# Performance work log

Measured on AMD Instinct MI355X. Metric: run time of the kernel, lower is better.

The kernel has to match this reference:

```python
import jax, jax.numpy as jnp
import numpy as np

EMBED, PDIM, HEADS, FFN = 192, 96, 8, 384
HID = int(2 * FFN / 3)                        # 256
CH = [HID - (HID // 4) * 3] + [HID // 4] * 3  # [64, 64, 64, 64]
SCALES = [1, 3, 5, 7]
B, H, W = 8, 128, 128


def conv2d(x, w, b=None, pad=0, groups=1):
    out = jax.lax.conv_general_dilated(
        x, w, (1, 1), [(pad, pad), (pad, pad)],
        feature_group_count=groups,
        dimension_numbers=('NCHW', 'OIHW', 'NCHW'))
    return out if b is None else out + b[None, :, None, None]


def layer_norm(x, g, b, eps=1e-6):
    m = x.mean(-1, keepdims=True)
    v = ((x - m) ** 2).mean(-1, keepdims=True)
    return (x - m) * jax.lax.rsqrt(v + eps) * g + b


def batch_norm(x, g, b, m, v, eps=1e-5):
    # eval-mode BatchNorm2d with running stats
    inv = jax.lax.rsqrt(v + eps)
    return (x - m[None, :, None, None]) * (g * inv)[None, :, None, None] + b[None, :, None, None]


def block_forward(x, p):
    # --- pos: depthwise 3x3 residual ---
    xc = x.transpose(0, 3, 1, 2)  # NCHW
    xc = xc + conv2d(xc, p['pos_w'], p['pos_b'], pad=1, groups=EMBED)

    # --- retention (ATK_SPA) branch ---
    y = layer_norm(xc.transpose(0, 2, 3, 1), p['ln1_g'], p['ln1_b'])
    yc = y.transpose(0, 3, 1, 2)
    b, c, h, w = yc.shape
    x1, x2 = yc[:, :PDIM], yc[:, PDIM:]
    qkv = conv2d(conv2d(x1, p['qkv_w']), p['qkv_dw_w'], pad=1, groups=3 * PDIM)
    q, k, v = jnp.split(qkv, 3, axis=1)
    cph = PDIM // HEADS
    rs = lambda t: t.reshape(b, HEADS, cph, h * w)
    q, k, v = rs(q), rs(k), rs(v)
    q = q / jnp.maximum(jnp.linalg.norm(q, axis=-1, keepdims=True), 1e-12)
    k = k / jnp.maximum(jnp.linalg.norm(k, axis=-1, keepdims=True), 1e-12)
    attn = jnp.einsum('bhcn,bhdn->bhcd', q, k) * p['temperature']  # [b,heads,cph,cph]
    # dynamic top-k from gate (int() truncation -> floor, value is positive)
    g1 = jax.nn.relu(conv2d(yc, p['gate_w1'], p['gate_b1']))
    gate = jax.nn.sigmoid(conv2d(g1, p['gate_w2'], p['gate_b2']))
    dyn_k = jnp.floor(cph * gate.mean())
    # rank-based top-k mask == scatter of topk indices (jit-safe for dynamic k)
    ranks = jnp.argsort(jnp.argsort(-attn, axis=-1), axis=-1)
    mask = ranks.astype(attn.dtype) < dyn_k
    attn = jax.nn.softmax(jnp.where(mask, attn, -jnp.inf), axis=-1)
    out = jnp.einsum('bhcd,bhdn->bhcn', attn, v)
    # out1..out4 are identical; weighted sum == single matmul scaled
    out = out * (p['attn1'] + p['attn2'] + p['attn3'] + p['attn4'])
    out = out.reshape(b, PDIM, h, w)
    out = conv2d(jnp.concatenate([out, x2], axis=1), p['proj_w'])
    xc = xc + out

    # --- FFN (HSSFGN) branch ---
    z = layer_norm(xc.transpose(0, 2, 3, 1), p['ln2_g'], p['ln2_b'])
    zc = z.transpose(0, 3, 1, 2)
    v0 = batch_norm(jax.nn.gelu(conv2d(zc, p['fc1_w']), approximate=False),
                    p['bn1_g'], p['bn1_b'], p['bn1_m'], p['bn1_v'])
    parts = jnp.split(v0, np.cumsum(CH[:-1]).tolist(), axis=1)
    dws = [conv2d(parts[i], p['dw%d_w' % i], p['dw%d_b' % i],
                  pad=SCALES[i] // 2, groups=CH[i]) for i in range(4)]
    u = jnp.concatenate(dws, axis=1) + v0
    u = batch_norm(jax.nn.gelu(u, approximate=False),
                   p['bn2_g'], p['bn2_b'], p['bn2_m'], p['bn2_v'])
    u = u * v0
    u = batch_norm(conv2d(u, p['fc2_w']),
                   p['bn3_g'], p['bn3_b'], p['bn3_m'], p['bn3_v'])
    xc = xc + u
    return xc.transpose(0, 2, 3, 1)


def setup_inputs() -> dict:
    ki = iter(jax.random.split(jax.random.key(0), 64))
    nrm = lambda shape, s=0.05: jax.random.normal(next(ki), shape, dtype=jnp.float32) * s
    inp = {
        'x': jax.random.normal(next(ki), (B, H, W, EMBED), dtype=jnp.float32),
        'pos_w': nrm((EMBED, 1, 3, 3)), 'pos_b': jnp.zeros((EMBED,)),
        'ln1_g': jnp.ones((EMBED,)), 'ln1_b': jnp.zeros((EMBED,)),
        'temperature': jnp.ones((HEADS, 1, 1)),
        'qkv_w': nrm((3 * PDIM, PDIM, 1, 1)),
        'qkv_dw_w': nrm((3 * PDIM, 1, 3, 3)),
        'proj_w': nrm((EMBED, EMBED, 1, 1)),
        'gate_w1': nrm((EMBED // 2, EMBED, 1, 1), 0.02), 'gate_b1': jnp.zeros((EMBED // 2,)),
        'gate_w2': nrm((1, EMBED // 2, 1, 1), 0.02), 'gate_b2': jnp.zeros((1,)),
        'attn1': jnp.full((1,), 0.2), 'attn2': jnp.full((1,), 0.2),
        'attn3': jnp.full((1,), 0.2), 'attn4': jnp.full((1,), 0.2),
        'ln2_g': jnp.ones((EMBED,)), 'ln2_b': jnp.zeros((EMBED,)),
        'fc1_w': nrm((HID, EMBED, 1, 1)),
        'bn1_g': jnp.ones((HID,)), 'bn1_b': jnp.zeros((HID,)),
        'bn1_m': jnp.zeros((HID,)), 'bn1_v': jnp.ones((HID,)),
        'bn2_g': jnp.ones((HID,)), 'bn2_b': jnp.zeros((HID,)),
        'bn2_m': jnp.zeros((HID,)), 'bn2_v': jnp.ones((HID,)),
        'fc2_w': nrm((EMBED, HID, 1, 1)),
        'bn3_g': jnp.ones((EMBED,)), 'bn3_b': jnp.zeros((EMBED,)),
        'bn3_m': jnp.zeros((EMBED,)), 'bn3_v': jnp.ones((EMBED,)),
    }
    for i in range(4):
        inp['dw%d_w' % i] = nrm((CH[i], 1, SCALES[i], SCALES[i]))
        inp['dw%d_b' % i] = jnp.zeros((CH[i],))
    return inp


def reference(x, pos_w, pos_b, ln1_g, ln1_b, temperature, qkv_w, qkv_dw_w, proj_w,
              gate_w1, gate_b1, gate_w2, gate_b2, attn1, attn2, attn3, attn4,
              ln2_g, ln2_b, fc1_w, bn1_g, bn1_b, bn1_m, bn1_v,
              dw0_w, dw0_b, dw1_w, dw1_b, dw2_w, dw2_b, dw3_w, dw3_b,
              bn2_g, bn2_b, bn2_m, bn2_v, fc2_w, bn3_g, bn3_b, bn3_m, bn3_v):
    p = dict(locals())
    xx = p.pop('x')
    return block_forward(xx, p)
```

## Files before the change

### kernel.cpp

```cpp
#include <hip/hip_runtime.h>
#include <hip/hip_bf16.h>
#include <math.h>

#define BB 8
#define HH 128
#define WW 128
#define HW (HH*WW)
#define NPIX (BB*HW)

typedef unsigned short u16;
typedef __attribute__((ext_vector_type(4))) float  floatx4;
typedef __attribute__((ext_vector_type(4))) short  short4v;
typedef __attribute__((ext_vector_type(8))) short  short8v;

static __device__ __forceinline__ float gelu_exact(float x){
    return 0.5f*x*(1.0f+erff(x*0.70710678118654752440f));
}
static __device__ __forceinline__ float b2f(u16 v){
    union { unsigned u; float f; } x; x.u = ((unsigned)v)<<16; return x.f;
}
static __device__ __forceinline__ u16 f2b(float f){
    __hip_bfloat16 h = __float2bfloat16(f);
    return *(u16*)&h;
}

#define WQ 27648
#define WP 36864
#define WG 18432
#define WF1 49152
#define WF2 49152
#define WTOT (WQ+WP+WG+WF1+WF2)
__global__ __launch_bounds__(256) void wprep_k(const float* __restrict__ a,
    const float* __restrict__ b, const float* __restrict__ c,
    const float* __restrict__ d, const float* __restrict__ e, u16* __restrict__ o)
{
    int i = blockIdx.x*256 + threadIdx.x;
    if (i >= WTOT) return;
    float v;
    if (i < WQ) v = a[i];
    else if (i < WQ+WP) v = b[i-WQ];
    else if (i < WQ+WP+WG) v = c[i-WQ-WP];
    else if (i < WQ+WP+WG+WF1) v = d[i-WQ-WP-WG];
    else v = e[i-WQ-WP-WG-WF1];
    o[i] = f2b(v);
}

__global__ __launch_bounds__(256) void pos_conv_k(const float* __restrict__ x,
    const float* __restrict__ w, const float* __restrict__ bias, u16* __restrict__ out)
{
    int bid = blockIdx.x;
    int sb = (bid & 7)*(gridDim.x >> 3) + (bid >> 3);
    int gid = sb*256 + threadIdx.x;
    int c4 = gid % 48; int rest = gid / 48;
    int seg = rest & 15; rest >>= 4;
    int hy = rest % HH; int b = rest / HH;
    int c0 = c4*4;
    float wr[3][3][4];
    #pragma unroll
    for (int j=0;j<4;j++)
        #pragma unroll
        for (int ky=0;ky<3;ky++)
            #pragma unroll
            for (int kx=0;kx<3;kx++)
                wr[ky][kx][j] = w[(c0+j)*9 + ky*3 + kx];
    float4 bias4 = *(const float4*)(bias + c0);
    const float4* x4 = (const float4*)x;
    const float4* r0 = x4 + ((size_t)(b*HH + hy-1)*WW)*48 + c4;
    const float4* r1 = x4 + ((size_t)(b*HH + hy  )*WW)*48 + c4;
    const float4* r2 = x4 + ((size_t)(b*HH + hy+1)*WW)*48 + c4;
    bool v0 = hy > 0, v2 = hy < HH-1;
    float4 z4 = make_float4(0.f,0.f,0.f,0.f);
    int s0 = seg*8;
    float4 cA[3], cB[3], cC[3], cP[3], cN[3];
    bool la = s0 > 0;
    cA[0] = (v0&&la) ? r0[(size_t)(s0-1)*48] : z4;
    cA[1] = la ? r1[(size_t)(s0-1)*48] : z4;
    cA[2] = (v2&&la) ? r2[(size_t)(s0-1)*48] : z4;
    cB[0] = v0 ? r0[(size_t)s0*48] : z4;  cB[1] = r1[(size_t)s0*48];  cB[2] = v2 ? r2[(size_t)s0*48] : z4;
    cC[0] = v0 ? r0[(size_t)(s0+1)*48] : z4; cC[1] = r1[(size_t)(s0+1)*48]; cC[2] = v2 ? r2[(size_t)(s0+1)*48] : z4;
    {
        bool ok = (s0+2) < WW;
        size_t off = (size_t)(s0+2)*48;
        cP[0] = (v0&&ok) ? r0[off] : z4;
        cP[1] = ok ? r1[off] : z4;
        cP[2] = (v2&&ok) ? r2[off] : z4;
    }
    u16* orow = out + ((size_t)(b*HH + hy)*WW)*192 + c0;
    for (int i2=0; i2<8; i2++){
        int wx = s0 + i2;
        bool okc = (wx+3) < WW;
        size_t noff = (size_t)(wx+3)*48;
        cN[0] = (v0 && okc) ? r0[noff] : z4;
        cN[1] = okc ? r1[noff] : z4;
        cN[2] = (v2 && okc) ? r2[noff] : z4;
        float4 acc = bias4;
        #pragma unroll
        for (int i=0;i<3;i++){
            acc.x = fmaf(wr[i][0][0], cA[i].x, acc.x);
            acc.y = fmaf(wr[i][0][1], cA[i].y, acc.y);
            acc.z = fmaf(wr[i][0][2], cA[i].z, acc.z);
            acc.w = fmaf(wr[i][0][3], cA[i].w, acc.w);
            acc.x = fmaf(wr[i][1][0], cB[i].x, acc.x);
            acc.y = fmaf(wr[i][1][1], cB[i].y, acc.y);
            acc.z = fmaf(wr[i][1][2], cB[i].z, acc.z);
            acc.w = fmaf(wr[i][1][3], cB[i].w, acc.w);
            acc.x = fmaf(wr[i][2][0], cC[i].x, acc.x);
            acc.y = fmaf(wr[i][2][1], cC[i].y, acc.y);
            acc.z = fmaf(wr[i][2][2], cC[i].z, acc.z);
            acc.w = fmaf(wr[i][2][3], cC[i].w, acc.w);
        }
        acc.x += cB[1].x; acc.y += cB[1].y; acc.z += cB[1].z; acc.w += cB[1].w;
        short4v o; o.x=(short)f2b(acc.x); o.y=(short)f2b(acc.y);
        o.z=(short)f2b(acc.z); o.w=(short)f2b(acc.w);
        *(short4v*)(orow + (size_t)wx*192) = o;
        #pragma unroll
        for (int i=0;i<3;i++){ cA[i]=cB[i]; cB[i]=cC[i]; cC[i]=cP[i]; cP[i]=cN[i]; }
    }
}

__global__ __launch_bounds__(256) void ln_k(const u16* __restrict__ in,
    const float* __restrict__ g, const float* __restrict__ bta, u16* __restrict__ out)
{
    int wid = threadIdx.x >> 6, lane = threadIdx.x & 63;
    size_t pix = (size_t)blockIdx.x*4 + wid;
    const u16* row = in + pix*192;
    float x0 = b2f(row[lane]), x1 = b2f(row[lane+64]), x2 = b2f(row[lane+128]);
    float s = x0+x1+x2;
    float q = x0*x0 + x1*x1 + x2*x2;
    #pragma unroll
    for (int off=32; off; off>>=1){ s += __shfl_xor(s,off,64); q += __shfl_xor(q,off,64); }
    float mean = s*(1.f/192.f);
    float var  = q*(1.f/192.f) - mean*mean;
    float inv  = rsqrtf(var + 1e-6f);
    u16* orow = out + pix*192;
    orow[lane]     = f2b((x0-mean)*inv*g[lane]     + bta[lane]);
    orow[lane+64]  = f2b((x1-mean)*inv*g[lane+64]  + bta[lane+64]);
    orow[lane+128] = f2b((x2-mean)*inv*g[lane+128] + bta[lane+128]);
}

#define GM_NONE 0
#define GM_RES 1
#define GM_GELU_BN 2
#define GM_BN_RES 3
#define GM_BIAS_RELU 4
#define WSTR 264

template<int MODE, int K, bool SPLIT=false>
__global__ __launch_bounds__(256) void gemm_bf16_k(
    const u16* __restrict__ A, int lda,
    const u16* __restrict__ A2, int lda2,
    const u16* __restrict__ W,
    void* __restrict__ Cv, int ldc,
    const u16* __restrict__ R, int ldr,
    const float* __restrict__ bg, const float* __restrict__ bb,
    const float* __restrict__ bm_, const float* __restrict__ bv,
    int N)
{
    __shared__ u16 Ws[64*WSTR];
    int t = threadIdx.x;
    int bn = blockIdx.x * 64;
    int bm = blockIdx.y * 256;
    {
        constexpr int KQ = K/4;
        int brow = t >> 2, bq = t & 3;
        int n = bn + brow;
        bool nv = n < N;
        const u16* src = W + (size_t)n*K + bq*KQ;
        #pragma unroll
        for (int j=0; j<KQ; j+=8){
            short8v v = {};
            if (nv) v = *(const short8v*)(src + j);
            *(short8v*)&Ws[brow*WSTR + bq*KQ + j] = v;
        }
    }
    __syncthreads();
    int wave = t >> 6, lane = t & 63;
    int wm = wave*64;
    int lr = lane & 15, lk = lane >> 4;
    const u16* arow  = A + (size_t)(bm + wm + lr)*lda + lk*8;
    const u16* arow2 = SPLIT ? (A2 + (size_t)(bm + wm + lr)*lda2 + lk*8) : nullptr;
    floatx4 acc[4][4] = {};
    #pragma unroll
    for (int k0 = 0; k0 < K; k0 += 32){
        short8v afr[4];
        if (SPLIT && k0 >= 96){
            #pragma unroll
            for (int m=0;m<4;m++)
                afr[m] = *(const short8v*)(arow2 + (size_t)(m*16)*lda2 + (k0-96));
        } else {
            #pragma unroll
            for (int m=0;m<4;m++)
                afr[m] = *(const short8v*)(arow + (size_t)(m*16)*lda + k0);
        }
        #pragma unroll
        for (int n2=0;n2<4;n2++){
            short8v bfr = *(const short8v*)&Ws[(n2*16+lr)*WSTR + k0 + lk*8];
            #pragma unroll
            for (int m=0;m<4;m++)
                acc[m][n2] = __builtin_amdgcn_mfma_f32_16x16x32_bf16(afr[m], bfr, acc[m][n2], 0,0,0);
        }
    }
    #pragma unroll
    for (int m=0;m<4;m++){
        #pragma unroll
        for (int n2=0;n2<4;n2++){
            int gcol = bn + n2*16 + lr;
            if (gcol >= N) continue;
            #pragma unroll
            for (int rg=0; rg<4; rg++){
                int grow = bm + wm + m*16 + lk*4 + rg;
                float v = acc[m][n2][rg];
                if (MODE == GM_RES){
                    v += b2f(R[(size_t)grow*ldr + gcol]);
                    ((u16*)Cv)[(size_t)grow*ldc + gcol] = f2b(v);
                } else if (MODE == GM_BN_RES){
                    float bnv = (v - bm_[gcol])*rsqrtf(bv[gcol]+1e-5f)*bg[gcol] + bb[gcol];
                    ((float*)Cv)[(size_t)grow*ldc + gcol] = bnv + b2f(R[(size_t)grow*ldr + gcol]);
                } else if (MODE == GM_GELU_BN){
                    float gl = gelu_exact(v);
                    v = (gl - bm_[gcol])*rsqrtf(bv[gcol]+1e-5f)*bg[gcol] + bb[gcol];
                    ((u16*)Cv)[(size_t)grow*ldc + gcol] = f2b(v);
                } else if (MODE == GM_BIAS_RELU){
                    ((u16*)Cv)[(size_t)grow*ldc + gcol] = f2b(fmaxf(v + bg[gcol], 0.f));
                } else {
                    ((u16*)Cv)[(size_t)grow*ldc + gcol] = f2b(v);
                }
            }
        }
    }
}

__global__ __launch_bounds__(256) void gate2_k(const u16* __restrict__ G1,
    const float* __restrict__ w2, const float* __restrict__ b2, float* __restrict__ gpix)
{
    int pix = blockIdx.x*256 + threadIdx.x;
    const short4v* g4 = (const short4v*)(G1 + (size_t)pix*96);
    const float4* w4 = (const float4*)w2;
    float s = b2[0];
    #pragma unroll
    for (int j=0;j<24;j++){
        short4v g = g4[j]; float4 w = w4[j];
        s += b2f((u16)g.x)*w.x + b2f((u16)g.y)*w.y + b2f((u16)g.z)*w.z + b2f((u16)g.w)*w.w;
    }
    gpix[pix] = 1.f/(1.f+expf(-s));
}

__global__ __launch_bounds__(1024) void gate_reduce_k(const float* __restrict__ gpix,
                                                      float* __restrict__ dynk)
{
    __shared__ float sm[16];
    float s = 0.f;
    for (int i=threadIdx.x; i<NPIX; i+=1024) s += gpix[i];
    #pragma unroll
    for (int off=32; off; off>>=1) s += __shfl_xor(s,off,64);
    int wid = threadIdx.x>>6, lane = threadIdx.x&63;
    if (lane==0) sm[wid]=s;
    __syncthreads();
    if (threadIdx.x==0){
        float tot=0.f; for (int i=0;i<16;i++) tot+=sm[i];
        *dynk = floorf(12.0f * (tot/(float)NPIX));
    }
}

#define QPOS(c8) ((c8)*8 + ((c8)>>2)*4)
#define QTAPSTRIDE 324
__global__ __launch_bounds__(256) void qkv_dw_k(const u16* __restrict__ in,
    const float* __restrict__ w, u16* __restrict__ out, size_t planeStride)
{
    __shared__ float wlds[9*QTAPSTRIDE];
    int t = threadIdx.x;
    for (int i=t; i<2592; i+=256){
        int tap = i/288, cc = i%288;
        wlds[tap*QTAPSTRIDE + QPOS(cc>>3) + (cc&7)] = w[cc*9+tap];
    }
    __syncthreads();
    int bid = blockIdx.x;
    int sb = (bid & 7)*(gridDim.x >> 3) + (bid >> 3);
    int idx = sb*256 + t;
    int c8 = idx % 36; int px2 = idx / 36;
    int wp = px2 & 63; int hy = (px2 >> 6) & 127; int img = px2 >> 13;
    int wx0 = wp*2;
    int c0 = c8*8;
    int wofs = QPOS(c8);
    float acc0[8] = {}, acc1[8] = {};
    #pragma unroll
    for (int ky=0; ky<3; ky++){
        int hh = hy + ky - 1; if ((unsigned)hh >= HH) continue;
        const u16* rowp = in + ((size_t)(img*HH+hh)*WW)*288 + c0;
        #pragma unroll
        for (int cc=0; cc<4; cc++){
            int cx = wx0 - 1 + cc;
            if ((unsigned)cx >= WW) continue;
            short8v v = *(const short8v*)(rowp + (size_t)cx*288);
            float vf[8];
            #pragma unroll
            for (int j=0;j<8;j++) vf[j] = b2f((u16)v[j]);
            if (cc < 3){
                floatx4 wa = *(const floatx4*)&wlds[(ky*3+cc)*QTAPSTRIDE + wofs];
                floatx4 wb = *(const floatx4*)&wlds[(ky*3+cc)*QTAPSTRIDE + wofs + 4];
                #pragma unroll
                for (int j=0;j<4;j++){ acc0[j]   = fmaf(wa[j], vf[j],   acc0[j]);
                                       acc0[4+j] = fmaf(wb[j], vf[4+j], acc0[4+j]); }
            }
            if (cc >= 1){
                floatx4 wa = *(const floatx4*)&wlds[(ky*3+cc-1)*QTAPSTRIDE + wofs];
                floatx4 wb = *(const floatx4*)&wlds[(ky*3+cc-1)*QTAPSTRIDE + wofs + 4];
                #pragma unroll
                for (int j=0;j<4;j++){ acc1[j]   = fmaf(wa[j], vf[j],   acc1[j]);
                                       acc1[4+j] = fmaf(wb[j], vf[4+j], acc1[4+j]); }
            }
        }
    }
    size_t pix0 = (size_t)(img*HH+hy)*WW + wx0;
    int sec = c0/96, qc0 = c0 - sec*96;
    u16* outp = out + (size_t)sec*planeStride + qc0;
    short8v o0, o1;
    #pragma unroll
    for (int j=0;j<8;j++){ o0[j] = (short)f2b(acc0[j]); o1[j] = (short)f2b(acc1[j]); }
    *(short8v*)(outp + pix0*96) = o0;
    *(short8v*)(outp + (pix0+1)*96) = o1;
}

__global__ __launch_bounds__(256) void gram_k(const u16* __restrict__ Qp,
    const u16* __restrict__ Kp, float* __restrict__ part)
{
    int bh = blockIdx.x;
    int slice = blockIdx.y;
    int img = bh >> 3, h = bh & 7;
    const u16* Qb = Qp + (size_t)img*HW*96 + h*12;
    const u16* Kb = Kp + (size_t)img*HW*96 + h*12;
    __shared__ float qs[64][12];
    __shared__ float ks[64][12];
    int t = threadIdx.x;
    float acc = 0.f;
    int c = (t<144) ? t/12 : (t<156 ? t-144 : t-156);
    int d = (t<144) ? t%12 : 0;
    for (int st=0; st<16; st++){
        int pix0 = slice*1024 + st*64;
        __syncthreads();
        for (int i=t; i<384; i+=256){
            int p = i/6, j = i%6;
            const u16* src = (j<3) ? (Qb + (size_t)(pix0+p)*96 + j*4)
                                   : (Kb + (size_t)(pix0+p)*96 + (j-3)*4);
            short4v v = *(const short4v*)src;
            float f0=b2f((u16)v.x), f1=b2f((u16)v.y), f2=b2f((u16)v.z), f3=b2f((u16)v.w);
            if (j<3){ int jj=j*4;     qs[p][jj]=f0; qs[p][jj+1]=f1; qs[p][jj+2]=f2; qs[p][jj+3]=f3; }
            else    { int jj=(j-3)*4; ks[p][jj]=f0; ks[p][jj+1]=f1; ks[p][jj+2]=f2; ks[p][jj+3]=f3; }
        }
        __syncthreads();
        if (t<144){        for (int p=0;p<64;p++) acc = fmaf(qs[p][c], ks[p][d], acc); }
        else if (t<156){   for (int p=0;p<64;p++) acc = fmaf(qs[p][c], qs[p][c], acc); }
        else if (t<168){   for (int p=0;p<64;p++) acc = fmaf(ks[p][c], ks[p][c], acc); }
    }
    if (t<168) part[((size_t)bh*16 + slice)*168 + t] = acc;
}

__global__ __launch_bounds__(256) void gram_combine_k(const float* __restrict__ part,
                                                      float* __restrict__ gram, int n)
{
    int i = blockIdx.x*256 + threadIdx.x;
    if (i >= n) return;
    int bh = i/168, t = i%168;
    float s = 0.f;
    for (int sl=0; sl<16; sl++) s += part[((size_t)bh*16+sl)*168 + t];
    gram[i] = s;
}

__global__ __launch_bounds__(256) void attn_k(const float* __restrict__ gram,
    const float* __restrict__ temp, const float* __restrict__ dynk_p,
    const float* __restrict__ a1, const float* __restrict__ a2,
    const float* __restrict__ a3, const float* __restrict__ a4,
    float* __restrict__ attnW)
{
    int bh = blockIdx.x;
    int h = bh & 7;
    __shared__ float av[12][12];
    __shared__ float mv[12][12];
    __shared__ float nq[12], nk[12];
    int t = threadIdx.x;
    if (t < 12) nq[t] = fmaxf(sqrtf(gram[bh*168+144+t]), 1e-12f);
    else if (t < 24) nk[t-12] = fmaxf(sqrtf(gram[bh*168+156+(t-12)]), 1e-12f);
    __syncthreads();
    if (t < 144){
        int c=t/12, d=t%12;
        av[c][d] = gram[bh*168+t] / (nq[c]*nk[d]) * temp[h];
    }
    __syncthreads();
    float dk = *dynk_p;
    if (t < 144){
        int c=t/12, d=t%12; float v = av[c][d];
        int r = 0;
        #pragma unroll
        for (int j=0;j<12;j++){
            float o = av[c][j];
            r += (o > v) ? 1 : ((o == v && j < d) ? 1 : 0);
        }
        mv[c][d] = ((float)r < dk) ? v : -INFINITY;
    }
    __syncthreads();
    if (t < 12){
        float mx = -INFINITY;
        for (int d2=0; d2<12; d2++) mx = fmaxf(mx, mv[t][d2]);
        float e[12]; float s = 0.f;
        for (int d2=0; d2<12; d2++){ e[d2] = expf(mv[t][d2]-mx); s += e[d2]; }
        float sc = (a1[0]+a2[0]+a3[0]+a4[0]) / s;
        for (int d2=0; d2<12; d2++) attnW[(size_t)bh*144 + t*12 + d2] = e[d2]*sc;
    }
}

__global__ __launch_bounds__(256) void attn_apply_k(const u16* __restrict__ Vp,
    const float* __restrict__ attnW, u16* __restrict__ P)
{
    int gid = blockIdx.x*256 + threadIdx.x;
    int h = gid % 8; size_t pix = (size_t)(gid / 8);
    int img = (int)(pix >> 14);
    const u16* vp = Vp + pix*96 + h*12;
    float vf[12];
    #pragma unroll
    for (int j=0;j<3;j++){
        short4v v = *(const short4v*)(vp + j*4);
        vf[j*4+0]=b2f((u16)v.x); vf[j*4+1]=b2f((u16)v.y);
        vf[j*4+2]=b2f((u16)v.z); vf[j*4+3]=b2f((u16)v.w);
    }
    const float* awb = attnW + ((size_t)(img*8+h))*144;
    u16 o[12];
    #pragma unroll
    for (int cc=0; cc<12; cc++){
        const float4* ap = (const float4*)(awb + cc*12);
        float4 a0 = ap[0], a1 = ap[1], a2 = ap[2];
        float s = a0.x*vf[0] + a0.y*vf[1] + a0.z*vf[2] + a0.w*vf[3]
                + a1.x*vf[4] + a1.y*vf[5] + a1.z*vf[6] + a1.w*vf[7]
                + a2.x*vf[8] + a2.y*vf[9] + a2.z*vf[10]+ a2.w*vf[11];
        o[cc] = f2b(s);
    }
    u16* op = P + pix*96 + h*12;
    *(short4v*)(op)   = *(short4v*)&o[0];
    *(short4v*)(op+4) = *(short4v*)&o[4];
    *(short4v*)(op+8) = *(short4v*)&o[8];
}

template<int KS>
__global__ __launch_bounds__(256) void ffn_dw_g(const u16* __restrict__ V0,
    const float* __restrict__ wsrc, const float* __restrict__ bsrc, int cbase,
    const float* __restrict__ bn2g, const float* __restrict__ bn2b,
    const float* __restrict__ bn2m, const float* __restrict__ bn2v,
    u16* __restrict__ U)
{
    constexpr int PAD = KS/2;
    __shared__ float wlds[KS*KS*64];
    __shared__ float bng[64], bnb[64], bnm[64], bnvr[64];
    int t = threadIdx.x;
    for (int i=t; i<KS*KS*64; i+=256){
        int tap = i >> 6, cc = i & 63;
        wlds[tap*64 + cc] = wsrc[cc*KS*KS + tap];
    }
    if (t < 64){
        bng[t] = bn2g[cbase+t]; bnb[t] = bn2b[cbase+t];
        bnm[t] = bn2m[cbase+t]; bnvr[t] = rsqrtf(bn2v[cbase+t]+1e-5f);
    }
    __syncthreads();
    int ci = t & 7, seg = t >> 3;
    int bid = blockIdx.x;
    int rowid = (bid & 7)*(gridDim.x >> 3) + (bid >> 3);
    int img = rowid >> 7, hy = rowid & 127;
    int c0r = ci*8;
    int c0 = cbase + c0r;
    int x0 = seg*4;
    float acc[4][8];
    {
        floatx4 b0 = *(const floatx4*)(bsrc + c0r);
        floatx4 b1 = *(const floatx4*)(bsrc + c0r + 4);
        #pragma unroll
        for (int dx=0;dx<4;dx++){
            #pragma unroll
            for (int j=0;j<4;j++){ acc[dx][j]=b0[j]; acc[dx][4+j]=b1[j]; }
        }
    }
    #pragma unroll
    for (int ky=0; ky<KS; ky++){
        int hh = hy + ky - PAD;
        if ((unsigned)hh >= HH) continue;
        float wr[KS][8];
        #pragma unroll
        for (int kx=0; kx<KS; kx++){
            floatx4 wa = *(const floatx4*)&wlds[(ky*KS+kx)*64 + c0r];
            floatx4 wb = *(const floatx4*)&wlds[(ky*KS+kx)*64 + c0r + 4];
            #pragma unroll
            for (int j=0;j<4;j++){ wr[kx][j]=wa[j]; wr[kx][4+j]=wb[j]; }
        }
        const u16* rowp = V0 + ((size_t)(img*HH+hh)*WW)*256 + c0;
        #pragma unroll
        for (int cc=0; cc<4+2*PAD; cc++){
            int cx = x0 - PAD + cc;
            if ((unsigned)cx >= WW) continue;
            short8v v = *(const short8v*)(rowp + (size_t)cx*256);
            float vf[8];
            #pragma unroll
            for (int j=0;j<8;j++) vf[j] = b2f((u16)v[j]);
            #pragma unroll
            for (int dx=0; dx<4; dx++){
                int kx = cc - dx;
                if (kx < 0 || kx >= KS) continue;
                #pragma unroll
                for (int j=0;j<8;j++) acc[dx][j] = fmaf(wr[kx][j], vf[j], acc[dx][j]);
            }
        }
    }
    size_t rbase = (size_t)(img*HH+hy)*WW;
    #pragma unroll
    for (int dx=0; dx<4; dx++){
        size_t pix = rbase + x0 + dx;
        short8v vc = *(const short8v*)(V0 + pix*256 + c0);
        short8v o;
        #pragma unroll
        for (int j=0;j<8;j++){
            float v0c = b2f((u16)vc[j]);
            float u1 = acc[dx][j] + v0c;
            float gl = gelu_exact(u1);
            float bn = (gl - bnm[c0r+j])*bnvr[c0r+j]*bng[c0r+j] + bnb[c0r+j];
            o[j] = (short)f2b(bn*v0c);
        }
        *(short8v*)(U + pix*256 + c0) = o;
    }
}

extern "C" void kernel_launch(void* const* d_in, const int* in_sizes, int n_in,
                              void* d_out, int out_size, void* d_ws, size_t ws_size,
                              hipStream_t stream)
{
    const float* x     = (const float*)d_in[0];
    const float* pos_w = (const float*)d_in[1];
    const float* pos_b = (const float*)d_in[2];
    const float* ln1g  = (const float*)d_in[3];
    const float* ln1b  = (const float*)d_in[4];
    const float* temp  = (const float*)d_in[5];
    const float* qkvw  = (const float*)d_in[6];
    const float* qkvdw = (const float*)d_in[7];
    const float* projw = (const float*)d_in[8];
    const float* gw1   = (const float*)d_in[9];
    const float* gb1   = (const float*)d_in[10];
    const float* gw2   = (const float*)d_in[11];
    const float* gb2   = (const float*)d_in[12];
    const float* a1    = (const float*)d_in[13];
    const float* a2    = (const float*)d_in[14];
    const float* a3    = (const float*)d_in[15];
    const float* a4    = (const float*)d_in[16];
    const float* ln2g  = (const float*)d_in[17];
    const float* ln2b  = (const float*)d_in[18];
    const float* fc1w  = (const float*)d_in[19];
    const float* bn1g  = (const float*)d_in[20];
    const float* bn1b  = (const float*)d_in[21];
    const float* bn1m  = (const float*)d_in[22];
    const float* bn1v  = (const float*)d_in[23];
    const float* bn2g  = (const float*)d_in[24];
    const float* bn2b  = (const float*)d_in[25];
    const float* bn2m  = (const float*)d_in[26];
    const float* bn2v  = (const float*)d_in[27];
    const float* fc2w  = (const float*)d_in[28];
    const float* bn3g  = (const float*)d_in[29];
    const float* bn3b  = (const float*)d_in[30];
    const float* bn3m  = (const float*)d_in[31];
    const float* bn3v  = (const float*)d_in[32];
    const float* dw0w  = (const float*)d_in[33];
    const float* dw0b  = (const float*)d_in[34];
    const float* dw1w  = (const float*)d_in[35];
    const float* dw1b  = (const float*)d_in[36];
    const float* dw2w  = (const float*)d_in[37];
    const float* dw2b  = (const float*)d_in[38];
    const float* dw3w  = (const float*)d_in[39];
    const float* dw3b  = (const float*)d_in[40];

    float* OUT = (float*)d_out;

    char* p = (char*)d_ws;
    float* gpix  = (float*)p;                 p += (size_t)NPIX*4;
    float* dynk  = (float*)p;                 p += 256;
    float* gpart = (float*)p;                 p += 64*16*168*4;
    float* gram  = (float*)p;                 p += 64*168*4;
    float* attnW = (float*)p;                 p += 64*144*4;
    u16*   wbf   = (u16*)p;                   p += (size_t)WTOT*2;
    u16*   Abf   = (u16*)p;                   p += (size_t)NPIX*192*2;
    size_t fixedB = (size_t)(p - (char*)d_ws);

    size_t perImg = (size_t)HW*2*(192+288+288);
    int CBr = 2;
    if (ws_size >= fixedB + 8*perImg) CBr = 8;
    else if (ws_size >= fixedB + 4*perImg) CBr = 4;
    int NCHUNKr = BB/CBr;
    size_t CHWr = (size_t)CBr*HW;

    u16* Ybf = (u16*)p;                   p += CHWr*192*2;
    u16* B1  = (u16*)p;                   p += CHWr*288*2;
    u16* B2  = (u16*)p;
    u16* qkvwb = wbf;
    u16* projwb= wbf + WQ;
    u16* gw1b  = wbf + WQ + WP;
    u16* fc1b  = wbf + WQ + WP + WG;
    u16* fc2b  = wbf + WQ + WP + WG + WF1;
    u16* G1bf  = B1;
    u16* QKVbf = B1;
    u16* QKVdbf= B2;
    u16* P96   = B1;
    u16* Zbf   = B2;
    u16* V0bf  = B1;
    u16* Ubf   = B2;

    wprep_k<<<(WTOT+255)/256, 256, 0, stream>>>(qkvw, projw, gw1, fc1w, fc2w, wbf);
    pos_conv_k<<<BB*HH*16*48/256, 256, 0, stream>>>(x, pos_w, pos_b, Abf);

    for (int c=0; c<NCHUNKr; c++){
        const u16* Ab = Abf + (size_t)c*CHWr*192;
        ln_k<<<CHWr/4, 256, 0, stream>>>(Ab, ln1g, ln1b, Ybf);
        dim3 g(2, CHWr/256);
        gemm_bf16_k<GM_BIAS_RELU,192><<<g, 256, 0, stream>>>(Ybf, 192, nullptr, 0,
            gw1b, G1bf, 96, nullptr, 0, gb1, nullptr, nullptr, nullptr, 96);
        gate2_k<<<CHWr/256, 256, 0, stream>>>(G1bf, gw2, gb2, gpix + (size_t)c*CHWr);
    }
    gate_reduce_k<<<1, 1024, 0, stream>>>(gpix, dynk);

    for (int c=0; c<NCHUNKr; c++){
        u16* Ab = Abf + (size_t)c*CHWr*192;
        if (NCHUNKr > 1)
            ln_k<<<CHWr/4, 256, 0, stream>>>(Ab, ln1g, ln1b, Ybf);
        {
            dim3 g(5, CHWr/256);
            gemm_bf16_k<GM_NONE,96><<<g, 256, 0, stream>>>(Ybf, 192, nullptr, 0,
                qkvwb, QKVbf, 288, nullptr, 0, nullptr,nullptr,nullptr,nullptr, 288);
        }
        size_t pstr = CHWr*96;
        qkv_dw_k<<<CHWr*18/256, 256, 0, stream>>>(QKVbf, qkvdw, QKVdbf, pstr);
        { dim3 g(CBr*8, 16); gram_k<<<g, 256, 0, stream>>>(QKVdbf, QKVdbf + pstr, gpart); }
        gram_combine_k<<<(CBr*8*168+255)/256, 256, 0, stream>>>(gpart, gram, CBr*8*168);
        attn_k<<<CBr*8, 256, 0, stream>>>(gram, temp, dynk, a1,a2,a3,a4, attnW);
        attn_apply_k<<<CHWr*8/256, 256, 0, stream>>>(QKVdbf + 2*pstr, attnW, P96);
        {
            dim3 g(3, CHWr/256);
            gemm_bf16_k<GM_RES,192,true><<<g, 256, 0, stream>>>(P96, 96, Ybf+96, 192,
                projwb, Ab, 192, Ab, 192, nullptr,nullptr,nullptr,nullptr, 192);
        }
        ln_k<<<CHWr/4, 256, 0, stream>>>(Ab, ln2g, ln2b, Zbf);
        {
            dim3 g(4, CHWr/256);
            gemm_bf16_k<GM_GELU_BN,192><<<g, 256, 0, stream>>>(Zbf, 192, nullptr, 0,
                fc1b, V0bf, 256, nullptr, 0, bn1g,bn1b,bn1m,bn1v, 256);
        }
        int rows = (int)(CHWr/WW);
        ffn_dw_g<1><<<rows, 256, 0, stream>>>(V0bf, dw0w, dw0b, 0,
            bn2g,bn2b,bn2m,bn2v, Ubf);
        ffn_dw_g<3><<<rows, 256, 0, stream>>>(V0bf, dw1w, dw1b, 64,
            bn2g,bn2b,bn2m,bn2v, Ubf);
        ffn_dw_g<5><<<rows, 256, 0, stream>>>(V0bf, dw2w, dw2b, 128,
            bn2g,bn2b,bn2m,bn2v, Ubf);
        ffn_dw_g<7><<<rows, 256, 0, stream>>>(V0bf, dw3w, dw3b, 192,
            bn2g,bn2b,bn2m,bn2v, Ubf);
        {
            dim3 g(3, CHWr/256);
            gemm_bf16_k<GM_BN_RES,256><<<g, 256, 0, stream>>>(Ubf, 256, nullptr, 0,
                fc2b, OUT + (size_t)c*CHWr*192, 192, Ab, 192, bn3g,bn3b,bn3m,bn3v, 192);
        }
    }
}
```

Before: 655.0 us.

## Rewrite pos conv as one-pixel-per-thread with transposed weights; swap GEMM grid axes

The depthwise 3x3 pos conv now assigns one output pixel's 4 channels to each thread, loading the 9 neighbours with clamped indices and masks. It reads weights from a tap-major transposed copy built in wprep_k, replacing the per-thread sliding window over 8 columns. This trades neighbour reuse in registers for more parallelism and simpler coalesced weight loads, at the cost of about 9x redundant input reads, which the cache may absorb. Separately, every GEMM launch swaps grid axes so the M tiles vary fastest, changing block scheduling order and how the shared weight tiles are reused in L2.

```diff
diff --git a/kernel.cpp b/kernel.cpp
--- a/kernel.cpp
+++ b/kernel.cpp
@@ -32,9 +32,13 @@
 #define WTOT (WQ+WP+WG+WF1+WF2)
 __global__ __launch_bounds__(256) void wprep_k(const float* __restrict__ a,
     const float* __restrict__ b, const float* __restrict__ c,
-    const float* __restrict__ d, const float* __restrict__ e, u16* __restrict__ o)
+    const float* __restrict__ d, const float* __restrict__ e,
+    const float* __restrict__ posw, u16* __restrict__ o, float* __restrict__ wT)
 {
     int i = blockIdx.x*256 + threadIdx.x;
+    if (i < 1728){
+        wT[i] = posw[(i%192)*9 + (i/192)];
+    }
     if (i >= WTOT) return;
     float v;
     if (i < WQ) v = a[i];
@@ -45,77 +49,61 @@
     o[i] = f2b(v);
 }
 
-__global__ __launch_bounds__(256) void pos_conv_k(const float* __restrict__ x,
-    const float* __restrict__ w, const float* __restrict__ bias, u16* __restrict__ out)
+__global__ __launch_bounds__(192) void pos_conv_k(const float* __restrict__ x,
+    const float* __restrict__ wT, const float* __restrict__ bias, u16* __restrict__ out)
 {
     int bid = blockIdx.x;
     int sb = (bid & 7)*(gridDim.x >> 3) + (bid >> 3);
-    int gid = sb*256 + threadIdx.x;
-    int c4 = gid % 48; int rest = gid / 48;
-    int seg = rest & 15; rest >>= 4;
-    int hy = rest % HH; int b = rest / HH;
+    int t = threadIdx.x;
+    int c4 = t % 48;
+    size_t pix = (size_t)sb*4 + (t/48);
+    int wx = (int)(pix % WW);
+    int hy = (int)((pix / WW) % HH);
+    int b  = (int)(pix / HW);
     int c0 = c4*4;
-    float wr[3][3][4];
-    #pragma unroll
-    for (int j=0;j<4;j++)
-        #pragma unroll
-        for (int ky=0;ky<3;ky++)
-            #pragma unroll
-            for (int kx=0;kx<3;kx++)
-                wr[ky][kx][j] = w[(c0+j)*9 + ky*3 + kx];
-    float4 bias4 = *(const float4*)(bias + c0);
+
+    int hcl[3], wcl[3];
+    float my[3], mx[3];
+    #pragma unroll
+    for (int i=0;i<3;i++){
+        int hh = hy + i - 1;
+        my[i] = ((unsigned)hh < HH) ? 1.f : 0.f;
+        hcl[i] = min(max(hh,0),HH-1);
+        int ww2 = wx + i - 1;
+        mx[i] = ((unsigned)ww2 < WW) ? 1.f : 0.f;
+        wcl[i] = min(max(ww2,0),WW-1);
+    }
     const float4* x4 = (const float4*)x;
-    const float4* r0 = x4 + ((size_t)(b*HH + hy-1)*WW)*48 + c4;
-    const float4* r1 = x4 + ((size_t)(b*HH + hy  )*WW)*48 + c4;
-    const float4* r2 = x4 + ((size_t)(b*HH + hy+1)*WW)*48 + c4;
-    bool v0 = hy > 0, v2 = hy < HH-1;
-    float4 z4 = make_float4(0.f,0.f,0.f,0.f);
-    int s0 = seg*8;
-    float4 cA[3], cB[3], cC[3], cP[3], cN[3];
-    bool la = s0 > 0;
-    cA[0] = (v0&&la) ? r0[(size_t)(s0-1)*48] : z4;
-    cA[1] = la ? r1[(size_t)(s0-1)*48] : z4;
-    cA[2] = (v2&&la) ? r2[(size_t)(s0-1)*48] : z4;
-    cB[0] = v0 ? r0[(size_t)s0*48] : z4;  cB[1] = r1[(size_t)s0*48];  cB[2] = v2 ? r2[(size_t)s0*48] : z4;
-    cC[0] = v0 ? r0[(size_t)(s0+1)*48] : z4; cC[1] = r1[(size_t)(s0+1)*48]; cC[2] = v2 ? r2[(size_t)(s0+1)*48] : z4;
-    {
-        bool ok = (s0+2) < WW;
-        size_t off = (size_t)(s0+2)*48;
-        cP[0] = (v0&&ok) ? r0[off] : z4;
-        cP[1] = ok ? r1[off] : z4;
-        cP[2] = (v2&&ok) ? r2[off] : z4;
-    }
-    u16* orow = out + ((size_t)(b*HH + hy)*WW)*192 + c0;
-    for (int i2=0; i2<8; i2++){
-        int wx = s0 + i2;
-        bool okc = (wx+3) < WW;
-        size_t noff = (size_t)(wx+3)*48;
-        cN[0] = (v0 && okc) ? r0[noff] : z4;
-        cN[1] = okc ? r1[noff] : z4;
-        cN[2] = (v2 && okc) ? r2[noff] : z4;
-        float4 acc = bias4;
-        #pragma unroll
-        for (int i=0;i<3;i++){
-            acc.x = fmaf(wr[i][0][0], cA[i].x, acc.x);
-            acc.y = fmaf(wr[i][0][1], cA[i].y, acc.y);
-            acc.z = fmaf(wr[i][0][2], cA[i].z, acc.z);
-            acc.w = fmaf(wr[i][0][3], cA[i].w, acc.w);
-            acc.x = fmaf(wr[i][1][0], cB[i].x, acc.x);
-            acc.y = fmaf(wr[i][1][1], cB[i].y, acc.y);
-            acc.z = fmaf(wr[i][1][2], cB[i].z, acc.z);
-            acc.w = fmaf(wr[i][1][3], cB[i].w, acc.w);
-            acc.x = fmaf(wr[i][2][0], cC[i].x, acc.x);
-            acc.y = fmaf(wr[i][2][1], cC[i].y, acc.y);
-            acc.z = fmaf(wr[i][2][2], cC[i].z, acc.z);
-            acc.w = fmaf(wr[i][2][3], cC[i].w, acc.w);
-        }
-        acc.x += cB[1].x; acc.y += cB[1].y; acc.z += cB[1].z; acc.w += cB[1].w;
-        short4v o; o.x=(short)f2b(acc.x); o.y=(short)f2b(acc.y);
-        o.z=(short)f2b(acc.z); o.w=(short)f2b(acc.w);
-        *(short4v*)(orow + (size_t)wx*192) = o;
-        #pragma unroll
-        for (int i=0;i<3;i++){ cA[i]=cB[i]; cB[i]=cC[i]; cC[i]=cP[i]; cP[i]=cN[i]; }
-    }
+    float4 xv[3][3];
+    #pragma unroll
+    for (int i=0;i<3;i++){
+        size_t rb = ((size_t)(b*HH + hcl[i])*WW)*48 + c4;
+        #pragma unroll
+        for (int k=0;k<3;k++)
+            xv[i][k] = x4[rb + (size_t)wcl[k]*48];
+    }
+    floatx4 wv[9];
+    #pragma unroll
+    for (int tap=0; tap<9; tap++)
+        wv[tap] = *(const floatx4*)&wT[tap*192 + c0];
+
+    float4 acc = *(const float4*)(bias + c0);
+    #pragma unroll
+    for (int i=0;i<3;i++){
+        #pragma unroll
+        for (int k=0;k<3;k++){
+            float m = my[i]*mx[k];
+            floatx4 w = wv[i*3+k];
+            acc.x = fmaf(w[0]*m, xv[i][k].x, acc.x);
+            acc.y = fmaf(w[1]*m, xv[i][k].y, acc.y);
+            acc.z = fmaf(w[2]*m, xv[i][k].z, acc.z);
+            acc.w = fmaf(w[3]*m, xv[i][k].w, acc.w);
+        }
+    }
+    acc.x += xv[1][1].x; acc.y += xv[1][1].y; acc.z += xv[1][1].z; acc.w += xv[1][1].w;
+    short4v o; o.x=(short)f2b(acc.x); o.y=(short)f2b(acc.y);
+    o.z=(short)f2b(acc.z); o.w=(short)f2b(acc.w);
+    *(short4v*)(out + pix*192 + c0) = o;
 }
 
 __global__ __launch_bounds__(256) void ln_k(const u16* __restrict__ in,
@@ -158,8 +146,8 @@
 {
     __shared__ u16 Ws[64*WSTR];
     int t = threadIdx.x;
-    int bn = blockIdx.x * 64;
-    int bm = blockIdx.y * 256;
+    int bn = blockIdx.y * 64;
+    int bm = blockIdx.x * 256;
     {
         constexpr int KQ = K/4;
         int brow = t >> 2, bq = t & 3;
@@ -578,6 +566,7 @@
     float* gpart = (float*)p;                 p += 64*16*168*4;
     float* gram  = (float*)p;                 p += 64*168*4;
     float* attnW = (float*)p;                 p += 64*144*4;
+    float* wposT = (float*)p;                 p += 1728*4;
     u16*   wbf   = (u16*)p;                   p += (size_t)WTOT*2;
     u16*   Abf   = (u16*)p;                   p += (size_t)NPIX*192*2;
     size_t fixedB = (size_t)(p - (char*)d_ws);
@@ -605,13 +594,14 @@
     u16* V0bf  = B1;
     u16* Ubf   = B2;
 
-    wprep_k<<<(WTOT+255)/256, 256, 0, stream>>>(qkvw, projw, gw1, fc1w, fc2w, wbf);
-    pos_conv_k<<<BB*HH*16*48/256, 256, 0, stream>>>(x, pos_w, pos_b, Abf);
+    wprep_k<<<(WTOT+255)/256, 256, 0, stream>>>(qkvw, projw, gw1, fc1w, fc2w,
+                                                pos_w, wbf, wposT);
+    pos_conv_k<<<NPIX/4, 192, 0, stream>>>(x, wposT, pos_b, Abf);
 
     for (int c=0; c<NCHUNKr; c++){
         const u16* Ab = Abf + (size_t)c*CHWr*192;
         ln_k<<<CHWr/4, 256, 0, stream>>>(Ab, ln1g, ln1b, Ybf);
-        dim3 g(2, CHWr/256);
+        dim3 g(CHWr/256, 2);
         gemm_bf16_k<GM_BIAS_RELU,192><<<g, 256, 0, stream>>>(Ybf, 192, nullptr, 0,
             gw1b, G1bf, 96, nullptr, 0, gb1, nullptr, nullptr, nullptr, 96);
         gate2_k<<<CHWr/256, 256, 0, stream>>>(G1bf, gw2, gb2, gpix + (size_t)c*CHWr);
@@ -623,7 +613,7 @@
         if (NCHUNKr > 1)
             ln_k<<<CHWr/4, 256, 0, stream>>>(Ab, ln1g, ln1b, Ybf);
         {
-            dim3 g(5, CHWr/256);
+            dim3 g(CHWr/256, 5);
             gemm_bf16_k<GM_NONE,96><<<g, 256, 0, stream>>>(Ybf, 192, nullptr, 0,
                 qkvwb, QKVbf, 288, nullptr, 0, nullptr,nullptr,nullptr,nullptr, 288);
         }
@@ -634,13 +624,13 @@
         attn_k<<<CBr*8, 256, 0, stream>>>(gram, temp, dynk, a1,a2,a3,a4, attnW);
         attn_apply_k<<<CHWr*8/256, 256, 0, stream>>>(QKVdbf + 2*pstr, attnW, P96);
         {
-            dim3 g(3, CHWr/256);
+            dim3 g(CHWr/256, 3);
             gemm_bf16_k<GM_RES,192,true><<<g, 256, 0, stream>>>(P96, 96, Ybf+96, 192,
                 projwb, Ab, 192, Ab, 192, nullptr,nullptr,nullptr,nullptr, 192);
         }
         ln_k<<<CHWr/4, 256, 0, stream>>>(Ab, ln2g, ln2b, Zbf);
         {
-            dim3 g(4, CHWr/256);
+            dim3 g(CHWr/256, 4);
             gemm_bf16_k<GM_GELU_BN,192><<<g, 256, 0, stream>>>(Zbf, 192, nullptr, 0,
                 fc1b, V0bf, 256, nullptr, 0, bn1g,bn1b,bn1m,bn1v, 256);
         }
@@ -654,7 +644,7 @@
         ffn_dw_g<7><<<rows, 256, 0, stream>>>(V0bf, dw3w, dw3b, 192,
             bn2g,bn2b,bn2m,bn2v, Ubf);
         {
-            dim3 g(3, CHWr/256);
+            dim3 g(CHWr/256, 3);
             gemm_bf16_k<GM_BN_RES,256><<<g, 256, 0, stream>>>(Ubf, 256, nullptr, 0,
                 fc2b, OUT + (size_t)c*CHWr*192, 192, Ab, 192, bn3g,bn3b,bn3m,bn3v, 192);
         }
```

After: 650.7 us. About the same (-0.7%).
